# Kernel optimization log

Measured on AMD Instinct MI355X. Metric: run time of the kernel, lower is better.

Reference implementation:

```python
import jax, jax.numpy as jnp
import numpy as np

DIM = 768
N_HEADS = 12
HEAD_DIM = DIM // N_HEADS
HIDDEN = int(DIM * 4.0)
EPS = 1e-6


def setup_inputs() -> dict:
    key = jax.random.key(0)
    ks = jax.random.split(key, 12)
    s = 0.02
    return {
        "x": jax.random.normal(ks[0], (4, 2048, DIM), dtype=jnp.float32),
        "ln1_g": jnp.ones((DIM,), jnp.float32),
        "ln1_b": jnp.zeros((DIM,), jnp.float32),
        "qkv_w": jax.random.normal(ks[1], (3 * DIM, DIM), jnp.float32) * s,
        "qkv_b": jnp.zeros((3 * DIM,), jnp.float32),
        "proj_w": jax.random.normal(ks[2], (DIM, DIM), jnp.float32) * s,
        "proj_b": jnp.zeros((DIM,), jnp.float32),
        "ln2_g": jnp.ones((DIM,), jnp.float32),
        "ln2_b": jnp.zeros((DIM,), jnp.float32),
        "fc1_w": jax.random.normal(ks[3], (HIDDEN, DIM), jnp.float32) * s,
        "fc1_b": jnp.zeros((HIDDEN,), jnp.float32),
        "fc2_w": jax.random.normal(ks[4], (DIM, HIDDEN), jnp.float32) * s,
        "fc2_b": jnp.zeros((DIM,), jnp.float32),
    }


def layer_norm(x, g, b):
    mu = jnp.mean(x, axis=-1, keepdims=True)
    var = jnp.mean(jnp.square(x - mu), axis=-1, keepdims=True)
    return (x - mu) * jax.lax.rsqrt(var + EPS) * g + b


def reference(x, ln1_g, ln1_b, qkv_w, qkv_b, proj_w, proj_b,
              ln2_g, ln2_b, fc1_w, fc1_b, fc2_w, fc2_b):
    B, N, D = x.shape
    # --- attention branch ---
    h = layer_norm(x, ln1_g, ln1_b)
    qkv = h @ qkv_w.T + qkv_b                      # [B, N, 3D]
    qkv = qkv.reshape(B, N, 3, N_HEADS, HEAD_DIM).transpose(2, 0, 3, 1, 4)
    q, k, v = qkv[0], qkv[1], qkv[2]               # each [B, H, N, d]
    scale = HEAD_DIM ** -0.5
    scores = jnp.einsum("bhqd,bhkd->bhqk", q, k) * scale
    attn = jax.nn.softmax(scores, axis=-1)
    out = jnp.einsum("bhqk,bhkd->bhqd", attn, v)   # [B, H, N, d]
    out = out.transpose(0, 2, 1, 3).reshape(B, N, D)
    x = x + (out @ proj_w.T + proj_b)
    # --- MLP branch ---
    h = layer_norm(x, ln2_g, ln2_b)
    h = jax.nn.gelu(h @ fc1_w.T + fc1_b, approximate=False)
    x = x + (h @ fc2_w.T + fc2_b)
    return x
```

## Files before the change

### kernel.cpp

```cpp
#include <hip/hip_runtime.h>


#define DIM    768
#define NHEAD  12
#define HDIM   64
#define HID    3072
#define BATCH  4
#define SEQ    2048
#define MTOT   (BATCH * SEQ)
#define D3     (3 * DIM)

#define QSCALE 0.18033688011112042f
#define GELU_K 2.30220816f

typedef short bf16x8 __attribute__((ext_vector_type(8)));
typedef float f32x4  __attribute__((ext_vector_type(4)));

__device__ __forceinline__ float exp2fast(float x) {
    return __builtin_amdgcn_exp2f(x);
}

__device__ __forceinline__ float gelu_f(float v) {
    float y = v * (1.f + 0.044715f * v * v) * GELU_K;
    float t = exp2fast(fminf(y, 30.f));
#if __has_builtin(__builtin_amdgcn_rcpf)
    return v * t * __builtin_amdgcn_rcpf(t + 1.f);
#else
    return v * t / (t + 1.f);
#endif
}

__device__ __forceinline__ short f2bf(float f) {
    union { float f; unsigned u; } c; c.f = f;
    unsigned r = c.u + 0x7FFFu + ((c.u >> 16) & 1u);
    return (short)(r >> 16);
}

__device__ __forceinline__ short4 pk4bf(float a, float b, float c, float d) {
    int lo, hi;
    asm("v_cvt_pk_bf16_f32 %0, %1, %2" : "=v"(lo) : "v"(a), "v"(b));
    asm("v_cvt_pk_bf16_f32 %0, %1, %2" : "=v"(hi) : "v"(c), "v"(d));
    short4 r;
    *(int*)&r.x = lo; *(int*)&r.z = hi;
    return r;
}

__device__ __forceinline__ void gld_lds16(const short* g, short* l) {
    __builtin_amdgcn_global_load_lds(
        (const __attribute__((address_space(1))) unsigned int*)g,
        (__attribute__((address_space(3))) unsigned int*)l, 16, 0, 0);
}

__global__ __launch_bounds__(256) void tobf4_k(
    const float* __restrict__ s0, short* __restrict__ d0, int n0,
    const float* __restrict__ s1, short* __restrict__ d1, int n1,
    const float* __restrict__ s2, short* __restrict__ d2, int n2,
    const float* __restrict__ s3, short* __restrict__ d3, int n3)
{
    int i = blockIdx.x * 256 + threadIdx.x;
    const float* s; short* d;
    if (i < n0)                { s = s0; d = d0; }
    else if ((i -= n0) < n1)   { s = s1; d = d1; }
    else if ((i -= n1) < n2)   { s = s2; d = d2; }
    else if ((i -= n2) < n3)   { s = s3; d = d3; }
    else return;
    float4 v = ((const float4*)s)[i];
    ((short4*)d)[i] = pk4bf(v.x, v.y, v.z, v.w);
}

__global__ __launch_bounds__(256) void ln_k(
    const float* __restrict__ x, const float* __restrict__ g,
    const float* __restrict__ bta, short* __restrict__ y)
{
    __shared__ float sb[2][4];
    const int row = blockIdx.x, tid = threadIdx.x;
    const float* xr = x + (size_t)row * DIM;
    float v0 = xr[tid], v1 = xr[tid + 256], v2 = xr[tid + 512];
    float s = v0 + v1 + v2;
    #pragma unroll
    for (int o = 32; o; o >>= 1) s += __shfl_down(s, o);
    if ((tid & 63) == 0) sb[0][tid >> 6] = s;
    __syncthreads();
    float mu = (sb[0][0] + sb[0][1] + sb[0][2] + sb[0][3]) * (1.f / DIM);
    float d0 = v0 - mu, d1 = v1 - mu, d2 = v2 - mu;
    float q = d0 * d0 + d1 * d1 + d2 * d2;
    #pragma unroll
    for (int o = 32; o; o >>= 1) q += __shfl_down(q, o);
    if ((tid & 63) == 0) sb[1][tid >> 6] = q;
    __syncthreads();
    float var = (sb[1][0] + sb[1][1] + sb[1][2] + sb[1][3]) * (1.f / DIM);
    float inv = rsqrtf(var + 1e-6f);
    short* yr = y + (size_t)row * DIM;
    yr[tid]       = f2bf(d0 * inv * g[tid]       + bta[tid]);
    yr[tid + 256] = f2bf(d1 * inv * g[tid + 256] + bta[tid + 256]);
    yr[tid + 512] = f2bf(d2 * inv * g[tid + 512] + bta[tid + 512]);
}

template<int MODE>
__global__ __launch_bounds__(512) void gemm8_k(
    const short* __restrict__ A, const short* __restrict__ W,
    const float* __restrict__ bias, const float* __restrict__ resid,
    void* __restrict__ Cout, short* __restrict__ vt,
    int M, int N, int K)
{
    __shared__ __align__(16) short sm[3][20480];

    const int tid = threadIdx.x, lane = tid & 63, wv = tid >> 6;
    const int l15 = lane & 15, quad = lane >> 4;

    const int gx = gridDim.x;
    const int bid = blockIdx.y * gx + blockIdx.x;
    const int s = bid >> 3, xcd = bid & 7;
    const int st = ((s >> 5) << 3) + xcd;
    const int cell = s & 31, cy = cell >> 2, cx = cell & 3;
    const int nstx = gx >> 2;
    const int sty = st / nstx, stx = st - sty * nstx;
    const int bm = (((sty << 3) + cy) << 7);
    const int bn = ((stx << 2) + cx) * 192;

    const int srow  = lane >> 3;
    const int chunk = (lane & 7) ^ srow;
    const int arow  = wv * 8 + srow;

    const short* Ag = A + (size_t)(bm + arow) * K + chunk * 8;
    const short* Wg = W + (size_t)(bn + arow) * K + chunk * 8;

    const int nt = K >> 6;

    auto stage = [&](short* s_, int k0) {
        #pragma unroll
        for (int i = 0; i < 2; ++i)
            gld_lds16(Ag + k0 + (size_t)(i * 64) * K,
                      s_ + i * 4096 + wv * 512);
        #pragma unroll
        for (int i = 0; i < 3; ++i)
            gld_lds16(Wg + k0 + (size_t)(i * 64) * K,
                      s_ + 8192 + i * 4096 + wv * 512);
    };

    f32x4 acc[4][3] = {};
    stage(&sm[0][0], 0);
    stage(&sm[1][0], (nt > 1 ? 1 : 0) << 6);

    const int rsel = (wv >> 2) * 64;
    const int csel = (wv & 3) * 48;
    const int xorr = (l15 & 7) << 4;

    for (int t = 0; t < nt; ++t) {
        const char* Sc = (const char*)&sm[t % 3][0];
        asm volatile("s_waitcnt vmcnt(5)" ::: "memory");
        __builtin_amdgcn_s_barrier();
        __builtin_amdgcn_sched_barrier(0);
        const int kn = (t + 2 < nt ? t + 2 : nt - 1) << 6;
        stage(&sm[(t + 2) % 3][0], kn);

        #pragma unroll
        for (int ks = 0; ks < 2; ++ks) {
            bf16x8 af[4], bfr[3];
            const int kc = ((ks << 6) + (quad << 4)) ^ xorr;
            #pragma unroll
            for (int mf = 0; mf < 4; ++mf) {
                const int row = rsel + mf * 16 + l15;
                af[mf] = *(const bf16x8*)(Sc + (row << 7) + kc);
            }
            #pragma unroll
            for (int nf = 0; nf < 3; ++nf) {
                const int brow = csel + nf * 16 + l15;
                bfr[nf] = *(const bf16x8*)(Sc + 16384 + (brow << 7) + kc);
            }
            __builtin_amdgcn_s_setprio(1);
            #pragma unroll
            for (int mf = 0; mf < 4; ++mf)
                #pragma unroll
                for (int nf = 0; nf < 3; ++nf)
                    acc[mf][nf] = __builtin_amdgcn_mfma_f32_16x16x32_bf16(
                        af[mf], bfr[nf], acc[mf][nf], 0, 0, 0);
            __builtin_amdgcn_s_setprio(0);
        }
    }

    if (MODE == 3 && bn >= 1536) {
        const size_t bbase = (size_t)(bm >> 11) * NHEAD;
        #pragma unroll
        for (int nf = 0; nf < 3; ++nf) {
            const int col = bn + csel + nf * 16 + l15;
            const float bv = bias[col];
            const int d = col - 1536, hh = d >> 6, dd = d & 63;
            const size_t vrow = (((bbase + hh) << 6) + dd) * SEQ;
            #pragma unroll
            for (int mf = 0; mf < 4; ++mf) {
                const int n0 = (bm & 2047) + rsel + mf * 16 + (quad << 2);
                *(short4*)&vt[vrow + n0] =
                    pk4bf(acc[mf][nf][0] + bv, acc[mf][nf][1] + bv,
                          acc[mf][nf][2] + bv, acc[mf][nf][3] + bv);
            }
        }
        return;
    }

    #pragma unroll
    for (int nf = 0; nf < 3; ++nf) {
        const int col = bn + csel + nf * 16 + l15;
        const float bv = bias[col];
        #pragma unroll
        for (int mf = 0; mf < 4; ++mf) {
            const int row0 = bm + rsel + mf * 16 + (quad << 2);
            #pragma unroll
            for (int r = 0; r < 4; ++r) {
                float v = acc[mf][nf][r] + bv;
                const size_t idx = (size_t)(row0 + r) * N + col;
                if (MODE == 0) {
                    ((float*)Cout)[idx] = v + resid[idx];
                } else if (MODE == 2) {
                    ((short*)Cout)[idx] = f2bf(gelu_f(v));
                } else {
                    if (col < DIM) v *= QSCALE;
                    ((short*)Cout)[idx] = f2bf(v);
                }
            }
        }
    }
}

__global__ __launch_bounds__(256) void attn_k(
    const short* __restrict__ qkv, const short* __restrict__ vt,
    short* __restrict__ out)
{
    __shared__ __align__(16) short Ks[64][64];
    __shared__ __align__(16) short Vs[64][64];
    __shared__ __align__(16) short Ps[4][32][64];

    const int bh = blockIdx.x, b = bh / NHEAD, h = bh % NHEAD;
    const int qb = blockIdx.y;
    const int tid = threadIdx.x, lane = tid & 63, wv = tid >> 6;
    const int l15 = lane & 15, quad = lane >> 4;
    const int lsw = (l15 & 7) << 3;

    const size_t qbase = (size_t)b * SEQ * D3;
    const size_t vbase = (((size_t)bh) << 6) * SEQ;

    bf16x8 qf[2][2];
    #pragma unroll
    for (int tm = 0; tm < 2; ++tm) {
        const int m = (qb << 7) + wv * 32 + tm * 16 + l15;
        #pragma unroll
        for (int ks = 0; ks < 2; ++ks)
            qf[tm][ks] = *(const bf16x8*)&qkv[qbase + (size_t)m * D3 + h * HDIM
                                             + ks * 32 + (quad << 3)];
    }

    float psum[2] = {0.f, 0.f};
    f32x4 acc[2][4] = {};

    const int srow = tid >> 3;
    const int scol = (tid & 7) << 3;

    for (int kb = 0; kb < SEQ / 64; ++kb) {
        __syncthreads();
        #pragma unroll
        for (int p = 0; p < 2; ++p) {
            const int r = srow + p * 32;
            const int pc = scol ^ ((r & 7) << 3);
            *(int4*)&Ks[r][pc] = *(const int4*)&qkv[qbase
                + (size_t)((kb << 6) + r) * D3 + DIM + h * HDIM + scol];
            *(int4*)&Vs[r][pc] = *(const int4*)&vt[vbase
                + (size_t)r * SEQ + (kb << 6) + scol];
        }
        __syncthreads();

        f32x4 st[2][4] = {};
        __builtin_amdgcn_s_setprio(1);
        #pragma unroll
        for (int kt = 0; kt < 4; ++kt)
            #pragma unroll
            for (int ks = 0; ks < 2; ++ks) {
                bf16x8 kf = *(const bf16x8*)
                    &Ks[kt * 16 + l15][(ks * 32 + (quad << 3)) ^ lsw];
                #pragma unroll
                for (int tm = 0; tm < 2; ++tm)
                    st[tm][kt] = __builtin_amdgcn_mfma_f32_16x16x32_bf16(
                        kf, qf[tm][ks], st[tm][kt], 0, 0, 0);
            }
        __builtin_amdgcn_s_setprio(0);

        #pragma unroll
        for (int tm = 0; tm < 2; ++tm) {
            #pragma unroll
            for (int kt = 0; kt < 4; ++kt) {
                const float p0 = exp2fast(st[tm][kt][0]);
                const float p1 = exp2fast(st[tm][kt][1]);
                const float p2 = exp2fast(st[tm][kt][2]);
                const float p3 = exp2fast(st[tm][kt][3]);
                psum[tm] += (p0 + p1) + (p2 + p3);
                *(short4*)&Ps[wv][tm * 16 + l15]
                             [(kt * 16 + (quad << 2)) ^ lsw] =
                    pk4bf(p0, p1, p2, p3);
            }
        }

        #pragma unroll
        for (int ks = 0; ks < 2; ++ks) {
            bf16x8 pf[2];
            #pragma unroll
            for (int tm = 0; tm < 2; ++tm)
                pf[tm] = *(const bf16x8*)
                    &Ps[wv][tm * 16 + l15][(ks * 32 + (quad << 3)) ^ lsw];
            __builtin_amdgcn_s_setprio(1);
            #pragma unroll
            for (int u = 0; u < 4; ++u) {
                bf16x8 vf = *(const bf16x8*)
                    &Vs[u * 16 + l15][(ks * 32 + (quad << 3)) ^ lsw];
                #pragma unroll
                for (int tm = 0; tm < 2; ++tm)
                    acc[tm][u] = __builtin_amdgcn_mfma_f32_16x16x32_bf16(
                        vf, pf[tm], acc[tm][u], 0, 0, 0);
            }
            __builtin_amdgcn_s_setprio(0);
        }
    }

    #pragma unroll
    for (int tm = 0; tm < 2; ++tm) {
        psum[tm] += __shfl_xor(psum[tm], 16);
        psum[tm] += __shfl_xor(psum[tm], 32);
    }

    #pragma unroll
    for (int tm = 0; tm < 2; ++tm) {
        const float inv = 1.f / psum[tm];
        const int q = (qb << 7) + wv * 32 + tm * 16 + l15;
        #pragma unroll
        for (int u = 0; u < 4; ++u) {
            const int d0 = u * 16 + (quad << 2);
            *(short4*)&out[((size_t)b * SEQ + q) * DIM + h * HDIM + d0] =
                pk4bf(acc[tm][u][0] * inv, acc[tm][u][1] * inv,
                      acc[tm][u][2] * inv, acc[tm][u][3] * inv);
        }
    }
}

extern "C" void kernel_launch(void* const* d_in, const int* in_sizes, int n_in,
                              void* d_out, int out_size, void* d_ws, size_t ws_size,
                              hipStream_t stream) {
    const float* x      = (const float*)d_in[0];
    const float* ln1_g  = (const float*)d_in[1];
    const float* ln1_b  = (const float*)d_in[2];
    const float* qkv_w  = (const float*)d_in[3];
    const float* qkv_b  = (const float*)d_in[4];
    const float* proj_w = (const float*)d_in[5];
    const float* proj_b = (const float*)d_in[6];
    const float* ln2_g  = (const float*)d_in[7];
    const float* ln2_b  = (const float*)d_in[8];
    const float* fc1_w  = (const float*)d_in[9];
    const float* fc1_b  = (const float*)d_in[10];
    const float* fc2_w  = (const float*)d_in[11];
    const float* fc2_b  = (const float*)d_in[12];
    float* out = (float*)d_out;

    short* ws16 = (short*)d_ws;
    short* wqkv = ws16;
    short* wprj = wqkv + (size_t)D3 * DIM;
    short* wf1  = wprj + (size_t)DIM * DIM;
    short* wf2  = wf1  + (size_t)HID * DIM;
    short* h    = wf2  + (size_t)DIM * HID;
    short* big  = h    + (size_t)MTOT * DIM;
    short* vtb  = big  + (size_t)MTOT * HID;
    float* x2   = (float*)(vtb + (size_t)MTOT * DIM);

    dim3 blk(256);

    const int n0 = (D3 * DIM) / 4, n1 = (DIM * DIM) / 4,
              n2 = (HID * DIM) / 4, n3 = (DIM * HID) / 4;
    tobf4_k<<<(n0 + n1 + n2 + n3 + 255) / 256, blk, 0, stream>>>(
        qkv_w, wqkv, n0, proj_w, wprj, n1, fc1_w, wf1, n2, fc2_w, wf2, n3);

    ln_k<<<MTOT, blk, 0, stream>>>(x, ln1_g, ln1_b, h);
    gemm8_k<3><<<dim3(D3 / 192, MTOT / 128), 512, 0, stream>>>(
        h, wqkv, qkv_b, nullptr, big, vtb, MTOT, D3, DIM);
    attn_k<<<dim3(BATCH * NHEAD, SEQ / 128), blk, 0, stream>>>(big, vtb, h);
    gemm8_k<0><<<dim3(DIM / 192, MTOT / 128), 512, 0, stream>>>(
        h, wprj, proj_b, x, x2, nullptr, MTOT, DIM, DIM);
    ln_k<<<MTOT, blk, 0, stream>>>(x2, ln2_g, ln2_b, vtb);
    gemm8_k<2><<<dim3(HID / 192, MTOT / 128), 512, 0, stream>>>(
        vtb, wf1, fc1_b, nullptr, big, nullptr, MTOT, HID, DIM);
    gemm8_k<0><<<dim3(DIM / 192, MTOT / 128), 512, 0, stream>>>(
        big, wf2, fc2_b, x2, out, nullptr, MTOT, DIM, HID);
}
```

Before: 366.1 us.

## Add 256x192-tile double-buffered GEMM for QKV and FC1 projections

Adds a new GEMM kernel with 256-row by 192-column output tiles, 24 accumulators per wave and double-buffered shared memory, and uses it for the QKV and FC1 projections. The original 128x192 triple-buffered kernel is kept only for the residual-add GEMMs. Larger tiles raise arithmetic intensity per byte loaded and halve the block count. In exchange they cost more registers and LDS per block, which may lower occupancy, and the XCD-aware block swizzle is dropped in the new kernel.

```diff
diff --git a/kernel.cpp b/kernel.cpp
--- a/kernel.cpp
+++ b/kernel.cpp
@@ -97,6 +97,123 @@
 }
 
 template<int MODE>
+__global__ __launch_bounds__(512) void gemmA_k(
+    const short* __restrict__ A, const short* __restrict__ W,
+    const float* __restrict__ bias,
+    void* __restrict__ Cout, short* __restrict__ vt,
+    int M, int N, int K)
+{
+    __shared__ __align__(16) short sm[2][28672];
+
+    const int tid = threadIdx.x, lane = tid & 63, wv = tid >> 6;
+    const int l15 = lane & 15, quad = lane >> 4;
+
+    const int gx = gridDim.x;
+    const int bid = blockIdx.y * gx + blockIdx.x;
+    const int bm = (bid / gx) << 8;
+    const int bn = (bid % gx) * 192;
+
+    const int srow  = lane >> 3;
+    const int chunk = (lane & 7) ^ srow;
+    const int arow  = wv * 8 + srow;
+
+    const short* Ag = A + (size_t)(bm + arow) * K + chunk * 8;
+    const short* Wg = W + (size_t)(bn + arow) * K + chunk * 8;
+
+    const int nt = K >> 6;
+
+    auto stage = [&](short* s_, int k0) {
+        #pragma unroll
+        for (int i = 0; i < 4; ++i)
+            gld_lds16(Ag + k0 + (size_t)(i * 64) * K,
+                      s_ + i * 4096 + wv * 512);
+        #pragma unroll
+        for (int i = 0; i < 3; ++i)
+            gld_lds16(Wg + k0 + (size_t)(i * 64) * K,
+                      s_ + 16384 + i * 4096 + wv * 512);
+    };
+
+    f32x4 acc[4][6] = {};
+    stage(&sm[0][0], 0);
+
+    const int rsel = (wv >> 1) * 64;
+    const int csel = (wv & 1) * 96;
+    const int xorr = (l15 & 7) << 4;
+
+    for (int t = 0; t < nt; ++t) {
+        const char* Sc = (const char*)&sm[t & 1][0];
+        asm volatile("s_waitcnt vmcnt(0)" ::: "memory");
+        __builtin_amdgcn_s_barrier();
+        __builtin_amdgcn_sched_barrier(0);
+        if (t + 1 < nt) stage(&sm[(t + 1) & 1][0], (t + 1) << 6);
+
+        #pragma unroll
+        for (int ks = 0; ks < 2; ++ks) {
+            bf16x8 af[4], bfr[6];
+            const int kc = ((ks << 6) + (quad << 4)) ^ xorr;
+            #pragma unroll
+            for (int mf = 0; mf < 4; ++mf) {
+                const int row = rsel + mf * 16 + l15;
+                af[mf] = *(const bf16x8*)(Sc + (row << 7) + kc);
+            }
+            #pragma unroll
+            for (int nf = 0; nf < 6; ++nf) {
+                const int brow = csel + nf * 16 + l15;
+                bfr[nf] = *(const bf16x8*)(Sc + 32768 + (brow << 7) + kc);
+            }
+            __builtin_amdgcn_s_setprio(1);
+            #pragma unroll
+            for (int mf = 0; mf < 4; ++mf)
+                #pragma unroll
+                for (int nf = 0; nf < 6; ++nf)
+                    acc[mf][nf] = __builtin_amdgcn_mfma_f32_16x16x32_bf16(
+                        af[mf], bfr[nf], acc[mf][nf], 0, 0, 0);
+            __builtin_amdgcn_s_setprio(0);
+        }
+    }
+
+    if (MODE == 3 && bn >= 1536) {
+        const size_t bbase = (size_t)(bm >> 11) * NHEAD;
+        #pragma unroll
+        for (int nf = 0; nf < 6; ++nf) {
+            const int col = bn + csel + nf * 16 + l15;
+            const float bv = bias[col];
+            const int d = col - 1536, hh = d >> 6, dd = d & 63;
+            const size_t vrow = (((bbase + hh) << 6) + dd) * SEQ;
+            #pragma unroll
+            for (int mf = 0; mf < 4; ++mf) {
+                const int n0 = (bm & 2047) + rsel + mf * 16 + (quad << 2);
+                *(short4*)&vt[vrow + n0] =
+                    pk4bf(acc[mf][nf][0] + bv, acc[mf][nf][1] + bv,
+                          acc[mf][nf][2] + bv, acc[mf][nf][3] + bv);
+            }
+        }
+        return;
+    }
+
+    #pragma unroll
+    for (int nf = 0; nf < 6; ++nf) {
+        const int col = bn + csel + nf * 16 + l15;
+        const float bv = bias[col];
+        #pragma unroll
+        for (int mf = 0; mf < 4; ++mf) {
+            const int row0 = bm + rsel + mf * 16 + (quad << 2);
+            #pragma unroll
+            for (int r = 0; r < 4; ++r) {
+                float v = acc[mf][nf][r] + bv;
+                const size_t idx = (size_t)(row0 + r) * N + col;
+                if (MODE == 2) {
+                    ((short*)Cout)[idx] = f2bf(gelu_f(v));
+                } else {
+                    if (col < DIM) v *= QSCALE;
+                    ((short*)Cout)[idx] = f2bf(v);
+                }
+            }
+        }
+    }
+}
+
+template<int MODE>
 __global__ __launch_bounds__(512) void gemm8_k(
     const short* __restrict__ A, const short* __restrict__ W,
     const float* __restrict__ bias, const float* __restrict__ resid,
@@ -179,25 +296,6 @@
         }
     }
 
-    if (MODE == 3 && bn >= 1536) {
-        const size_t bbase = (size_t)(bm >> 11) * NHEAD;
-        #pragma unroll
-        for (int nf = 0; nf < 3; ++nf) {
-            const int col = bn + csel + nf * 16 + l15;
-            const float bv = bias[col];
-            const int d = col - 1536, hh = d >> 6, dd = d & 63;
-            const size_t vrow = (((bbase + hh) << 6) + dd) * SEQ;
-            #pragma unroll
-            for (int mf = 0; mf < 4; ++mf) {
-                const int n0 = (bm & 2047) + rsel + mf * 16 + (quad << 2);
-                *(short4*)&vt[vrow + n0] =
-                    pk4bf(acc[mf][nf][0] + bv, acc[mf][nf][1] + bv,
-                          acc[mf][nf][2] + bv, acc[mf][nf][3] + bv);
-            }
-        }
-        return;
-    }
-
     #pragma unroll
     for (int nf = 0; nf < 3; ++nf) {
         const int col = bn + csel + nf * 16 + l15;
@@ -209,14 +307,7 @@
             for (int r = 0; r < 4; ++r) {
                 float v = acc[mf][nf][r] + bv;
                 const size_t idx = (size_t)(row0 + r) * N + col;
-                if (MODE == 0) {
-                    ((float*)Cout)[idx] = v + resid[idx];
-                } else if (MODE == 2) {
-                    ((short*)Cout)[idx] = f2bf(gelu_f(v));
-                } else {
-                    if (col < DIM) v *= QSCALE;
-                    ((short*)Cout)[idx] = f2bf(v);
-                }
+                ((float*)Cout)[idx] = v + resid[idx];
             }
         }
     }
@@ -375,14 +466,14 @@
         qkv_w, wqkv, n0, proj_w, wprj, n1, fc1_w, wf1, n2, fc2_w, wf2, n3);
 
     ln_k<<<MTOT, blk, 0, stream>>>(x, ln1_g, ln1_b, h);
-    gemm8_k<3><<<dim3(D3 / 192, MTOT / 128), 512, 0, stream>>>(
-        h, wqkv, qkv_b, nullptr, big, vtb, MTOT, D3, DIM);
+    gemmA_k<3><<<dim3(D3 / 192, MTOT / 256), 512, 0, stream>>>(
+        h, wqkv, qkv_b, big, vtb, MTOT, D3, DIM);
     attn_k<<<dim3(BATCH * NHEAD, SEQ / 128), blk, 0, stream>>>(big, vtb, h);
     gemm8_k<0><<<dim3(DIM / 192, MTOT / 128), 512, 0, stream>>>(
         h, wprj, proj_b, x, x2, nullptr, MTOT, DIM, DIM);
     ln_k<<<MTOT, blk, 0, stream>>>(x2, ln2_g, ln2_b, vtb);
-    gemm8_k<2><<<dim3(HID / 192, MTOT / 128), 512, 0, stream>>>(
-        vtb, wf1, fc1_b, nullptr, big, nullptr, MTOT, HID, DIM);
+    gemmA_k<2><<<dim3(HID / 192, MTOT / 256), 512, 0, stream>>>(
+        vtb, wf1, fc1_b, big, nullptr, MTOT, HID, DIM);
     gemm8_k<0><<<dim3(DIM / 192, MTOT / 128), 512, 0, stream>>>(
         big, wf2, fc2_b, x2, out, nullptr, MTOT, DIM, HID);
 }
```

After: 354.4 us. 3.2% less time.
